# Kernel tuning notes

Measured on AMD Instinct MI355X. Metric: run time of the kernel, lower is better.

Reference implementation:

```python
import jax, jax.numpy as jnp
import numpy as np

S, D, M, K, H = 4096, 768, 1024, 32, 8
DH = D // H  # 96
CTX = 10
EPS_LN = 1e-5
EPS_COS = 1e-8


def setup_inputs() -> dict:
    key = jax.random.key(0)
    ks = jax.random.split(key, 30)
    sc = 0.02
    n = lambda k, shp: jax.random.normal(k, shp, jnp.float32) * sc
    inp = {
        "text_embeddings": jax.random.normal(ks[0], (1, S, D), jnp.float32),
        "candidate_embeddings": jax.random.normal(ks[1], (M, K, D), jnp.float32),
        "mention_starts": jax.random.randint(ks[2], (M,), 0, S - 16),
        "span_lengths": jax.random.randint(ks[3], (M,), 0, 8),
        # relik_reader: Linear(2D->D), ReLU, Linear(D->1)
        "relik_w1": n(ks[4], (2 * D, D)), "relik_b1": jnp.zeros((D,), jnp.float32),
        "relik_w2": n(ks[5], (D, 1)), "relik_b2": jnp.zeros((1,), jnp.float32),
        # TransformerEncoderLayer (post-norm, relu, nhead=8, ffn=4D)
        "wq": n(ks[6], (D, D)), "bq": jnp.zeros((D,), jnp.float32),
        "wk": n(ks[7], (D, D)), "bk": jnp.zeros((D,), jnp.float32),
        "wv": n(ks[8], (D, D)), "bv": jnp.zeros((D,), jnp.float32),
        "wo": n(ks[9], (D, D)), "bo": jnp.zeros((D,), jnp.float32),
        "ln1_g": jnp.ones((D,), jnp.float32), "ln1_b": jnp.zeros((D,), jnp.float32),
        "ffn_w1": n(ks[10], (D, 4 * D)), "ffn_b1": jnp.zeros((4 * D,), jnp.float32),
        "ffn_w2": n(ks[11], (4 * D, D)), "ffn_b2": jnp.zeros((D,), jnp.float32),
        "ln2_g": jnp.ones((D,), jnp.float32), "ln2_b": jnp.zeros((D,), jnp.float32),
        # unirel_interaction: Linear(2D->D), ReLU, Linear(D->D)
        "uni_w1": n(ks[12], (2 * D, D)), "uni_b1": jnp.zeros((D,), jnp.float32),
        "uni_w2": n(ks[13], (D, D)), "uni_b2": jnp.zeros((D,), jnp.float32),
    }
    return inp


def _ln(x, g, b):
    mu = jnp.mean(x, -1, keepdims=True)
    var = jnp.mean(jnp.square(x - mu), -1, keepdims=True)
    return (x - mu) * jax.lax.rsqrt(var + EPS_LN) * g + b


def reference(text_embeddings, candidate_embeddings, mention_starts, span_lengths,
              relik_w1, relik_b1, relik_w2, relik_b2,
              wq, bq, wk, bk, wv, bv, wo, bo,
              ln1_g, ln1_b, ffn_w1, ffn_b1, ffn_w2, ffn_b2, ln2_g, ln2_b,
              uni_w1, uni_b1, uni_w2, uni_b2):
    txt = text_embeddings[0]                               # [S, D]
    seq = txt.shape[0]
    csum = jnp.concatenate([jnp.zeros((1, txt.shape[1]), txt.dtype),
                            jnp.cumsum(txt, axis=0)], axis=0)  # [S+1, D]
    ends = mention_starts + span_lengths
    # mean over [start, end] inclusive
    m_len = (span_lengths + 1).astype(txt.dtype)
    mention = (csum[ends + 1] - csum[mention_starts]) / m_len[:, None]  # [M, D]
    # context mean over [c_start, c_end) exclusive, as in original slicing
    c_start = jnp.maximum(0, mention_starts - CTX)
    c_end = jnp.minimum(seq - 1, ends + CTX)
    ctx = (csum[c_end] - csum[c_start]) / (c_end - c_start).astype(txt.dtype)[:, None]

    cand = candidate_embeddings                            # [M, K, D]
    mk = jnp.broadcast_to(mention[:, None, :], cand.shape) # [M, K, D]

    # relik score: MLP on [mention; candidate]
    cat_mc = jnp.concatenate([mk, cand], axis=-1)          # [M, K, 2D]
    h = jax.nn.relu(cat_mc @ relik_w1 + relik_b1)
    relik = (h @ relik_w2 + relik_b2)[..., 0]              # [M, K]

    # 2-token transformer encoder layer over stack([mention, candidate])
    x = jnp.stack([mk, cand], axis=2)                      # [M, K, 2, D]
    q = (x @ wq + bq).reshape(M, K, 2, H, DH)
    k_ = (x @ wk + bk).reshape(M, K, 2, H, DH)
    v = (x @ wv + bv).reshape(M, K, 2, H, DH)
    scores = jnp.einsum("mkqhd,mkvhd->mkhqv", q, k_) / jnp.sqrt(jnp.float32(DH))
    attn = jax.nn.softmax(scores, axis=-1)
    o = jnp.einsum("mkhqv,mkvhd->mkqhd", attn, v).reshape(M, K, 2, D)
    x1 = _ln(x + (o @ wo + bo), ln1_g, ln1_b)
    f = jax.nn.relu(x1 @ ffn_w1 + ffn_b1) @ ffn_w2 + ffn_b2
    x2 = _ln(x1 + f, ln2_g, ln2_b)                         # [M, K, 2, D]
    e0, e1 = x2[..., 0, :], x2[..., 1, :]
    n0 = jnp.maximum(jnp.linalg.norm(e0, axis=-1), EPS_COS)
    n1 = jnp.maximum(jnp.linalg.norm(e1, axis=-1), EPS_COS)
    atg = jnp.sum(e0 * e1, axis=-1) / (n0 * n1)            # [M, K]

    # unirel: MLP on [context; candidate], sigmoid of mean
    ck = jnp.broadcast_to(ctx[:, None, :], cand.shape)
    cat_cc = jnp.concatenate([ck, cand], axis=-1)
    inter = jax.nn.relu(cat_cc @ uni_w1 + uni_b1) @ uni_w2 + uni_b2
    unirel = jax.nn.sigmoid(jnp.mean(inter, axis=-1))      # [M, K]

    return jnp.stack([relik, atg, unirel], axis=0)         # [3, M, K]
```

## Files before the change

### kernel.cpp

```cpp
#include <hip/hip_runtime.h>
#include <math.h>

#define S_LEN 4096
#define D_DIM 768
#define M_CNT 1024
#define K_CNT 32
#define MK_CNT 32768
#define DH_DIM 96
#define CTX_W 10

typedef __bf16 bf16_t;
typedef bf16_t bf16x8 __attribute__((ext_vector_type(8)));
typedef float f32x4 __attribute__((ext_vector_type(4)));
typedef float f32x16 __attribute__((ext_vector_type(16)));
typedef int i32x4 __attribute__((ext_vector_type(4)));
typedef int i32x8 __attribute__((ext_vector_type(8)));

__device__ __forceinline__ float block_reduce_sum(float v, float* sbuf) {
#pragma unroll
    for (int off = 32; off; off >>= 1) v += __shfl_down(v, off);
    __syncthreads();
    int wave = threadIdx.x >> 6;
    int lane = threadIdx.x & 63;
    if (lane == 0) sbuf[wave] = v;
    __syncthreads();
    return sbuf[0] + sbuf[1] + sbuf[2] + sbuf[3];
}

template<int OUT_BF16, int RELU>
__global__ __launch_bounds__(256, 2) void gemm_mfma(
    const bf16_t* __restrict__ A, const bf16_t* __restrict__ Bt,
    const float* __restrict__ bias, void* __restrict__ C,
    int Kd, int N, int nx, int ny)
{
    __shared__ bf16_t As[128 * 64];
    __shared__ bf16_t Bs[128 * 64];
    const int tid = threadIdx.x;
    const int w = tid >> 6, l = tid & 63;
    int per = 8 * nx;
    int g = blockIdx.x / per, rr = blockIdx.x % per;
    int gs = ny - g * 8; if (gs > 8) gs = 8;
    const int row0 = (g * 8 + rr % gs) * 128, col0 = (rr / gs) * 128;

    const int srow = w * 8 + (l >> 3);
    const int gchunk = (l & 7) ^ ((l >> 3) & 7);
    const bf16_t* gA = A + (size_t)(row0 + srow) * Kd + gchunk * 8;
    const bf16_t* gB = Bt + (size_t)(col0 + srow) * Kd + gchunk * 8;

    const int wm = w >> 1, wn = w & 1;
    f32x4 acc[4][4] = {};

    for (int k0 = 0; k0 < Kd; k0 += 64) {
#pragma unroll
        for (int c = 0; c < 4; ++c) {
            __builtin_amdgcn_global_load_lds(
                (const __attribute__((address_space(1))) void*)(gA + (size_t)(c * 32) * Kd + k0),
                (__attribute__((address_space(3))) void*)(As + (c * 256 + w * 64) * 8), 16, 0, 0);
            __builtin_amdgcn_global_load_lds(
                (const __attribute__((address_space(1))) void*)(gB + (size_t)(c * 32) * Kd + k0),
                (__attribute__((address_space(3))) void*)(Bs + (c * 256 + w * 64) * 8), 16, 0, 0);
        }
        __syncthreads();
#pragma unroll
        for (int ks = 0; ks < 2; ++ks) {
            bf16x8 af[4], bfr[4];
#pragma unroll
            for (int i = 0; i < 4; ++i) {
                int arow = wm * 64 + i * 16 + (l & 15);
                int slot = (ks * 4 + (l >> 4)) ^ (l & 7);
                af[i] = *(const bf16x8*)(As + arow * 64 + slot * 8);
                int brow = wn * 64 + i * 16 + (l & 15);
                bfr[i] = *(const bf16x8*)(Bs + brow * 64 + slot * 8);
            }
#pragma unroll
            for (int i = 0; i < 4; ++i)
#pragma unroll
                for (int j = 0; j < 4; ++j)
                    acc[i][j] = __builtin_amdgcn_mfma_f32_16x16x32_bf16(af[i], bfr[j], acc[i][j], 0, 0, 0);
        }
        __syncthreads();
    }

#pragma unroll
    for (int i = 0; i < 4; ++i) {
        int row = row0 + wm * 64 + i * 16 + (l >> 4) * 4;
#pragma unroll
        for (int j = 0; j < 4; ++j) {
            int col = col0 + wn * 64 + j * 16 + (l & 15);
            float bv = bias ? bias[col] : 0.f;
#pragma unroll
            for (int r = 0; r < 4; ++r) {
                float v = acc[i][j][r] + bv;
                if (RELU) v = fmaxf(v, 0.f);
                if (OUT_BF16) ((bf16_t*)C)[(size_t)(row + r) * N + col] = (bf16_t)v;
                else          ((float*)C)[(size_t)(row + r) * N + col] = v;
            }
        }
    }
}

static inline void launch_gemm(const bf16_t* A, const bf16_t* Bt, const float* bias, void* C,
                               int rows, int Kd, int N, bool relu, bool outbf, hipStream_t st) {
    int nx = N / 128, ny = rows / 128;
    dim3 grid(nx * ny);
    if (outbf) {
        if (relu) gemm_mfma<1, 1><<<grid, 256, 0, st>>>(A, Bt, bias, C, Kd, N, nx, ny);
        else      gemm_mfma<1, 0><<<grid, 256, 0, st>>>(A, Bt, bias, C, Kd, N, nx, ny);
    } else {
        if (relu) gemm_mfma<0, 1><<<grid, 256, 0, st>>>(A, Bt, bias, C, Kd, N, nx, ny);
        else      gemm_mfma<0, 0><<<grid, 256, 0, st>>>(A, Bt, bias, C, Kd, N, nx, ny);
    }
}

template<int OMODE, int RELU>
__global__ __launch_bounds__(256, 2) void gemm_fp8(
    const unsigned char* __restrict__ A, const unsigned char* __restrict__ Bt,
    const float* __restrict__ bias, void* __restrict__ C,
    int Kd, int N, int nx, int ny)
{
    __shared__ unsigned char As[128 * 128];
    __shared__ unsigned char Bs[128 * 128];
    const int tid = threadIdx.x;
    const int w = tid >> 6, l = tid & 63;
    int per = 8 * nx;
    int g = blockIdx.x / per, rrb = blockIdx.x % per;
    int gs = ny - g * 8; if (gs > 8) gs = 8;
    const int row0 = (g * 8 + rrb % gs) * 128, col0 = (rrb / gs) * 128;
    const int wm = w >> 1, wn = w & 1;
    const int SA = 0x7F7F7F7F;

    const int srow = w * 8 + (l >> 3);
    const int gch = (l & 7) ^ ((l >> 3) & 7);
    const unsigned char* gA = A + (size_t)(row0 + srow) * Kd + gch * 16;
    const unsigned char* gB = Bt + (size_t)(col0 + srow) * Kd + gch * 16;

    f32x16 acc[2][2] = {};

    for (int k0 = 0; k0 < Kd; k0 += 128) {
#pragma unroll
        for (int q = 0; q < 4; ++q) {
            __builtin_amdgcn_global_load_lds(
                (const __attribute__((address_space(1))) void*)(gA + (size_t)(q * 32) * Kd + k0),
                (__attribute__((address_space(3))) void*)(As + (q * 256 + w * 64) * 16), 16, 0, 0);
            __builtin_amdgcn_global_load_lds(
                (const __attribute__((address_space(1))) void*)(gB + (size_t)(q * 32) * Kd + k0),
                (__attribute__((address_space(3))) void*)(Bs + (q * 256 + w * 64) * 16), 16, 0, 0);
        }
        __syncthreads();
#pragma unroll
        for (int s = 0; s < 2; ++s) {
            i32x8 af[2], bfr[2];
            int cb = s * 4 + ((l >> 5) << 1);
#pragma unroll
            for (int i = 0; i < 2; ++i) {
                int row = wm * 64 + i * 32 + (l & 31);
                int sl0 = cb ^ (row & 7);
                int sl1 = (cb + 1) ^ (row & 7);
                i32x4 lo = *(const i32x4*)(As + (row * 8 + sl0) * 16);
                i32x4 hi = *(const i32x4*)(As + (row * 8 + sl1) * 16);
                i32x8 a;
                a[0] = lo[0]; a[1] = lo[1]; a[2] = lo[2]; a[3] = lo[3];
                a[4] = hi[0]; a[5] = hi[1]; a[6] = hi[2]; a[7] = hi[3];
                af[i] = a;
                int colr = wn * 64 + i * 32 + (l & 31);
                int tl0 = cb ^ (colr & 7);
                int tl1 = (cb + 1) ^ (colr & 7);
                lo = *(const i32x4*)(Bs + (colr * 8 + tl0) * 16);
                hi = *(const i32x4*)(Bs + (colr * 8 + tl1) * 16);
                i32x8 b;
                b[0] = lo[0]; b[1] = lo[1]; b[2] = lo[2]; b[3] = lo[3];
                b[4] = hi[0]; b[5] = hi[1]; b[6] = hi[2]; b[7] = hi[3];
                bfr[i] = b;
            }
#pragma unroll
            for (int i = 0; i < 2; ++i)
#pragma unroll
                for (int j = 0; j < 2; ++j)
                    acc[i][j] = __builtin_amdgcn_mfma_scale_f32_32x32x64_f8f6f4(
                        af[i], bfr[j], acc[i][j], 0, 0, 0, SA, 0, SA);
        }
        __syncthreads();
    }

#pragma unroll
    for (int i = 0; i < 2; ++i) {
        int rbase = row0 + wm * 64 + i * 32 + 4 * (l >> 5);
#pragma unroll
        for (int j = 0; j < 2; ++j) {
            int col = col0 + wn * 64 + j * 32 + (l & 31);
            float bv = bias ? bias[col] : 0.f;
#pragma unroll
            for (int reg = 0; reg < 16; ++reg) {
                int row = rbase + (reg & 3) + 8 * (reg >> 2);
                float v = acc[i][j][reg] + bv;
                if (RELU) v = fmaxf(v, 0.f);
                if (OMODE == 1)
                    ((unsigned char*)C)[(size_t)row * N + col] =
                        (unsigned char)(__builtin_amdgcn_cvt_pk_fp8_f32(v, v, 0, false) & 0xff);
                else if (OMODE == 2)
                    ((bf16_t*)C)[(size_t)row * N + col] = (bf16_t)v;
                else
                    ((float*)C)[(size_t)row * N + col] = v;
            }
        }
    }
}

template<int OMODE, int RELU>
static inline void launch_fp8_t(const unsigned char* A, const unsigned char* Bt, const float* bias,
                                void* C, int rows, int Kd, int N, hipStream_t st) {
    int nx = N / 128, ny = rows / 128;
    gemm_fp8<OMODE, RELU><<<dim3(nx * ny), 256, 0, st>>>(A, Bt, bias, C, Kd, N, nx, ny);
}

__global__ __launch_bounds__(256) void transpose_bf16(
    const float* __restrict__ W, bf16_t* __restrict__ Wt, int Kd, int N)
{
    __shared__ float t[32][33];
    int bx = blockIdx.x * 32, by = blockIdx.y * 32;
    int x = threadIdx.x & 31, y = threadIdx.x >> 5;
#pragma unroll
    for (int yy = y; yy < 32; yy += 8) t[yy][x] = W[(size_t)(by + yy) * N + bx + x];
    __syncthreads();
#pragma unroll
    for (int yy = y; yy < 32; yy += 8) Wt[(size_t)(bx + yy) * Kd + by + x] = (bf16_t)t[x][yy];
}

__global__ __launch_bounds__(256) void transpose_fp8(
    const float* __restrict__ W, unsigned char* __restrict__ Wt, int Kd, int N)
{
    __shared__ float t[32][33];
    int bx = blockIdx.x * 32, by = blockIdx.y * 32;
    int x = threadIdx.x & 31, y = threadIdx.x >> 5;
#pragma unroll
    for (int yy = y; yy < 32; yy += 8) t[yy][x] = W[(size_t)(by + yy) * N + bx + x];
    __syncthreads();
    int xg = threadIdx.x & 7, yo = threadIdx.x >> 3;
    int lo = __builtin_amdgcn_cvt_pk_fp8_f32(t[xg * 4 + 0][yo], t[xg * 4 + 1][yo], 0, false);
    int both = __builtin_amdgcn_cvt_pk_fp8_f32(t[xg * 4 + 2][yo], t[xg * 4 + 3][yo], lo, true);
    *(int*)(Wt + (size_t)(bx + yo) * Kd + by + xg * 4) = both;
}

__global__ __launch_bounds__(256) void cvt_bf16(
    const float* __restrict__ x, bf16_t* __restrict__ y, int n4)
{
    int i = blockIdx.x * 256 + threadIdx.x;
    if (i < n4) {
        float4 v = ((const float4*)x)[i];
        bf16_t o4[4] = {(bf16_t)v.x, (bf16_t)v.y, (bf16_t)v.z, (bf16_t)v.w};
        ((uint2*)y)[i] = *(uint2*)o4;
    }
}

__global__ __launch_bounds__(256) void pack_bias5(
    const float* __restrict__ bq, const float* __restrict__ bk,
    const float* __restrict__ bv, float* __restrict__ o)
{
    int i = blockIdx.x * 256 + threadIdx.x;
    if (i >= 3840) return;
    float v = 0.f;
    if (i < 768) v = bq[i];
    else if (i < 1536) v = bk[i - 768];
    else if (i < 2304) v = bv[i - 1536];
    o[i] = v;
}

__global__ __launch_bounds__(256) void spans_kernel(
    const float* __restrict__ txt, const int* __restrict__ starts,
    const int* __restrict__ lens, float* __restrict__ mention,
    bf16_t* __restrict__ mentionb, bf16_t* __restrict__ ctxb)
{
    int m = blockIdx.x;
    int st = starts[m], ln = lens[m];
    int en = st + ln;
    int cs = st - CTX_W; if (cs < 0) cs = 0;
    int ce = en + CTX_W; if (ce > S_LEN - 1) ce = S_LEN - 1;
    int c = threadIdx.x;
    float s0 = 0.f, s1 = 0.f, s2 = 0.f;
    for (int r = st; r <= en; ++r) {
        const float* tr = txt + (size_t)r * D_DIM;
        s0 += tr[c]; s1 += tr[c + 256]; s2 += tr[c + 512];
    }
    float inv = 1.f / (float)(ln + 1);
    float* mp = mention + (size_t)m * D_DIM;
    bf16_t* mb = mentionb + (size_t)m * D_DIM;
    mp[c] = s0 * inv; mp[c + 256] = s1 * inv; mp[c + 512] = s2 * inv;
    mb[c] = (bf16_t)(s0 * inv); mb[c + 256] = (bf16_t)(s1 * inv); mb[c + 512] = (bf16_t)(s2 * inv);

    s0 = 0.f; s1 = 0.f; s2 = 0.f;
    for (int r = cs; r < ce; ++r) {
        const float* tr = txt + (size_t)r * D_DIM;
        s0 += tr[c]; s1 += tr[c + 256]; s2 += tr[c + 512];
    }
    inv = 1.f / (float)(ce - cs);
    bf16_t* cp = ctxb + (size_t)m * D_DIM;
    cp[c] = (bf16_t)(s0 * inv); cp[c + 256] = (bf16_t)(s1 * inv); cp[c + 512] = (bf16_t)(s2 * inv);
}

__global__ __launch_bounds__(256) void w2bar_kernel(
    const float* __restrict__ uni_w2, const float* __restrict__ uni_b2,
    float* __restrict__ w2bar, float* __restrict__ b2bar)
{
    __shared__ float sbuf[4];
    int d = blockIdx.x;
    float s = 0.f;
    if (d < D_DIM) {
        for (int j = threadIdx.x; j < D_DIM; j += 256) s += uni_w2[(size_t)d * D_DIM + j];
        s = block_reduce_sum(s, sbuf);
        if (threadIdx.x == 0) w2bar[d] = s * (1.f / (float)D_DIM);
    } else {
        for (int j = threadIdx.x; j < D_DIM; j += 256) s += uni_b2[j];
        s = block_reduce_sum(s, sbuf);
        if (threadIdx.x == 0) *b2bar = s * (1.f / (float)D_DIM);
    }
}

__global__ __launch_bounds__(512) void attn_kernel(
    const bf16_t* __restrict__ qkvm, const bf16_t* __restrict__ qkvc,
    bf16_t* __restrict__ o, int g0)
{
    int lc = blockIdx.x;
    int gg = g0 + lc;
    int m = gg >> 5;
    int h = threadIdx.x >> 6;
    int lane = threadIdx.x & 63;
    const bf16_t* bm = qkvm + (size_t)m * 3840 + h * DH_DIM;
    const bf16_t* bc = qkvc + (size_t)lc * 3840 + h * DH_DIM;

    float s00 = 0.f, s01 = 0.f, s10 = 0.f, s11 = 0.f;
    for (int d = lane; d < DH_DIM; d += 64) {
        float qmv = (float)bm[d], kmv = (float)bm[d + 768];
        float qcv = (float)bc[d], kcv = (float)bc[d + 768];
        s00 += qmv * kmv; s01 += qmv * kcv; s10 += qcv * kmv; s11 += qcv * kcv;
    }
#pragma unroll
    for (int off = 32; off; off >>= 1) {
        s00 += __shfl_down(s00, off); s01 += __shfl_down(s01, off);
        s10 += __shfl_down(s10, off); s11 += __shfl_down(s11, off);
    }
    s00 = __shfl(s00, 0); s01 = __shfl(s01, 0);
    s10 = __shfl(s10, 0); s11 = __shfl(s11, 0);
    const float sc = 0.1020620726159658f;
    s00 *= sc; s01 *= sc; s10 *= sc; s11 *= sc;
    float m0 = fmaxf(s00, s01), m1 = fmaxf(s10, s11);
    float e00 = expf(s00 - m0), e01 = expf(s01 - m0);
    float e10 = expf(s10 - m1), e11 = expf(s11 - m1);
    float i0 = 1.f / (e00 + e01), i1 = 1.f / (e10 + e11);
    float a00 = e00 * i0, a01 = e01 * i0, a10 = e10 * i1, a11 = e11 * i1;

    bf16_t* o0 = o + ((size_t)lc * 2) * D_DIM + h * DH_DIM;
    bf16_t* o1 = o0 + D_DIM;
    for (int d = lane; d < DH_DIM; d += 64) {
        float vmv = (float)bm[d + 1536], vcv = (float)bc[d + 1536];
        o0[d] = (bf16_t)(a00 * vmv + a01 * vcv);
        o1[d] = (bf16_t)(a10 * vmv + a11 * vcv);
    }
}

__global__ __launch_bounds__(256) void ln1_kernel(
    const bf16_t* __restrict__ x1pre, const float* __restrict__ mention,
    const bf16_t* __restrict__ candb, const float* __restrict__ g,
    const float* __restrict__ b, bf16_t* __restrict__ x1f,
    unsigned char* __restrict__ x1q, int g0)
{
    __shared__ float sbuf[4];
    int r = blockIdx.x;
    int lc = r >> 1, pos = r & 1;
    int gg = g0 + lc, m = gg >> 5;
    int c = threadIdx.x;
    float r0, r1, r2;
    if (pos) {
        const bf16_t* xr = candb + (size_t)gg * D_DIM;
        r0 = (float)xr[c]; r1 = (float)xr[c + 256]; r2 = (float)xr[c + 512];
    } else {
        const float* xr = mention + (size_t)m * D_DIM;
        r0 = xr[c]; r1 = xr[c + 256]; r2 = xr[c + 512];
    }
    const bf16_t* pr = x1pre + (size_t)r * D_DIM;
    float v0 = r0 + (float)pr[c];
    float v1 = r1 + (float)pr[c + 256];
    float v2 = r2 + (float)pr[c + 512];
    float mu = block_reduce_sum(v0 + v1 + v2, sbuf) * (1.f / (float)D_DIM);
    float d0 = v0 - mu, d1 = v1 - mu, d2 = v2 - mu;
    float var = block_reduce_sum(d0 * d0 + d1 * d1 + d2 * d2, sbuf) * (1.f / (float)D_DIM);
    float inv = rsqrtf(var + 1e-5f);
    float o0 = d0 * inv * g[c] + b[c];
    float o1 = d1 * inv * g[c + 256] + b[c + 256];
    float o2 = d2 * inv * g[c + 512] + b[c + 512];
    bf16_t* fp = x1f + (size_t)r * D_DIM;
    fp[c] = (bf16_t)o0; fp[c + 256] = (bf16_t)o1; fp[c + 512] = (bf16_t)o2;
    unsigned char* qp = x1q + (size_t)r * D_DIM;
    qp[c] = (unsigned char)(__builtin_amdgcn_cvt_pk_fp8_f32(o0, o0, 0, false) & 0xff);
    qp[c + 256] = (unsigned char)(__builtin_amdgcn_cvt_pk_fp8_f32(o1, o1, 0, false) & 0xff);
    qp[c + 512] = (unsigned char)(__builtin_amdgcn_cvt_pk_fp8_f32(o2, o2, 0, false) & 0xff);
}

__global__ __launch_bounds__(256) void heads_kernel(
    const bf16_t* __restrict__ x1f, const bf16_t* __restrict__ x2f,
    const float* __restrict__ g2, const float* __restrict__ b2g,
    const float* __restrict__ Ar, const float* __restrict__ Au,
    const bf16_t* __restrict__ qkvc, const float* __restrict__ rw2,
    const float* __restrict__ rb2, const float* __restrict__ w2bar,
    const float* __restrict__ b2bar, float* __restrict__ out, int g0)
{
    __shared__ float sbuf[4];
    int lc = blockIdx.x;
    int gg = g0 + lc, m = gg >> 5;
    int c = threadIdx.x;
    float e[2][3];
#pragma unroll
    for (int rr = 0; rr < 2; ++rr) {
        const bf16_t* x1 = x1f + (size_t)(2 * lc + rr) * D_DIM;
        const bf16_t* x2 = x2f + (size_t)(2 * lc + rr) * D_DIM;
        float v0 = (float)x1[c] + (float)x2[c];
        float v1 = (float)x1[c + 256] + (float)x2[c + 256];
        float v2 = (float)x1[c + 512] + (float)x2[c + 512];
        float mu = block_reduce_sum(v0 + v1 + v2, sbuf) * (1.f / (float)D_DIM);
        float d0 = v0 - mu, d1 = v1 - mu, d2 = v2 - mu;
        float var = block_reduce_sum(d0 * d0 + d1 * d1 + d2 * d2, sbuf) * (1.f / (float)D_DIM);
        float inv = rsqrtf(var + 1e-5f);
        e[rr][0] = d0 * inv * g2[c] + b2g[c];
        e[rr][1] = d1 * inv * g2[c + 256] + b2g[c + 256];
        e[rr][2] = d2 * inv * g2[c + 512] + b2g[c + 512];
    }
    float dd = e[0][0] * e[1][0] + e[0][1] * e[1][1] + e[0][2] * e[1][2];
    float aa = e[0][0] * e[0][0] + e[0][1] * e[0][1] + e[0][2] * e[0][2];
    float bb = e[1][0] * e[1][0] + e[1][1] * e[1][1] + e[1][2] * e[1][2];
    dd = block_reduce_sum(dd, sbuf);
    aa = block_reduce_sum(aa, sbuf);
    bb = block_reduce_sum(bb, sbuf);
    const float* ar = Ar + (size_t)m * D_DIM;
    const bf16_t* br = qkvc + (size_t)lc * 3840 + 2304;
    float rs = fmaxf(ar[c] + (float)br[c], 0.f) * rw2[c]
             + fmaxf(ar[c + 256] + (float)br[c + 256], 0.f) * rw2[c + 256]
             + fmaxf(ar[c + 512] + (float)br[c + 512], 0.f) * rw2[c + 512];
    rs = block_reduce_sum(rs, sbuf);
    const float* au = Au + (size_t)m * D_DIM;
    const bf16_t* bu = qkvc + (size_t)lc * 3840 + 3072;
    float us = fmaxf(au[c] + (float)bu[c], 0.f) * w2bar[c]
             + fmaxf(au[c + 256] + (float)bu[c + 256], 0.f) * w2bar[c + 256]
             + fmaxf(au[c + 512] + (float)bu[c + 512], 0.f) * w2bar[c + 512];
    us = block_reduce_sum(us, sbuf);
    if (threadIdx.x == 0) {
        float n0 = fmaxf(sqrtf(aa), 1e-8f);
        float n1 = fmaxf(sqrtf(bb), 1e-8f);
        out[MK_CNT + gg] = dd / (n0 * n1);
        out[gg] = rs + rb2[0];
        float z = us + *b2bar;
        out[2 * MK_CNT + gg] = 1.f / (1.f + expf(-z));
    }
}

extern "C" void kernel_launch(void* const* d_in, const int* in_sizes, int n_in,
                              void* d_out, int out_size, void* d_ws, size_t ws_size,
                              hipStream_t stream) {
    const float* text     = (const float*)d_in[0];
    const float* cand     = (const float*)d_in[1];
    const int*   starts   = (const int*)d_in[2];
    const int*   lens     = (const int*)d_in[3];
    const float* relik_w1 = (const float*)d_in[4];
    const float* relik_b1 = (const float*)d_in[5];
    const float* relik_w2 = (const float*)d_in[6];
    const float* relik_b2 = (const float*)d_in[7];
    const float* wq = (const float*)d_in[8];
    const float* bq = (const float*)d_in[9];
    const float* wk = (const float*)d_in[10];
    const float* bk = (const float*)d_in[11];
    const float* wv = (const float*)d_in[12];
    const float* bv = (const float*)d_in[13];
    const float* wo = (const float*)d_in[14];
    const float* bo = (const float*)d_in[15];
    const float* ln1_g = (const float*)d_in[16];
    const float* ln1_b = (const float*)d_in[17];
    const float* ffn_w1 = (const float*)d_in[18];
    const float* ffn_b1 = (const float*)d_in[19];
    const float* ffn_w2 = (const float*)d_in[20];
    const float* ffn_b2 = (const float*)d_in[21];
    const float* ln2_g = (const float*)d_in[22];
    const float* ln2_b = (const float*)d_in[23];
    const float* uni_w1 = (const float*)d_in[24];
    const float* uni_b1 = (const float*)d_in[25];
    const float* uni_w2 = (const float*)d_in[26];
    const float* uni_b2 = (const float*)d_in[27];
    float* out = (float*)d_out;

    const size_t MD = (size_t)M_CNT * D_DIM;
    const size_t DD = (size_t)D_DIM * D_DIM;

    size_t fixed_f = 21300000;
    int NC = 32768;
    while (NC > 128 && (fixed_f + (size_t)NC * 6912) * 4 > ws_size) NC >>= 1;
    const size_t NCD = (size_t)NC * D_DIM;

    float* p = (float*)d_ws;
    float* mention = p; p += MD;
    float* Ar      = p; p += MD;
    float* Au      = p; p += MD;
    float* bqkv5   = p; p += 3840;
    float* w2bar   = p; p += 768;
    float* b2bar   = p; p += 64;
    bf16_t* mentionb = (bf16_t*)p; p += MD / 2;
    bf16_t* ctxb     = (bf16_t*)p; p += MD / 2;
    bf16_t* qkvm     = (bf16_t*)p; p += (size_t)M_CNT * 3840 / 2;
    bf16_t* wcandT   = (bf16_t*)p; p += (size_t)3840 * 768 / 2;
    bf16_t* woT      = (bf16_t*)p; p += DD / 2;
    bf16_t* relikAT  = (bf16_t*)p; p += DD / 2;
    bf16_t* uniAT    = (bf16_t*)p; p += DD / 2;
    unsigned char* w1q = (unsigned char*)p; p += (size_t)3072 * 768 / 4;
    unsigned char* w2q = (unsigned char*)p; p += (size_t)3072 * 768 / 4;
    bf16_t* candb    = (bf16_t*)p; p += (size_t)MK_CNT * D_DIM / 2;
    bf16_t* qkvcb = (bf16_t*)p; p += (size_t)NC * 3840 / 2;
    bf16_t* obuf  = (bf16_t*)p; p += 2 * NCD / 2;
    bf16_t* x1pre = (bf16_t*)p; p += 2 * NCD / 2;
    bf16_t* x1f   = (bf16_t*)p; p += 2 * NCD / 2;
    bf16_t* x2f   = (bf16_t*)p; p += 2 * NCD / 2;
    unsigned char* x1q = (unsigned char*)p; p += 2 * NCD / 4;
    unsigned char* hb  = (unsigned char*)p; p += (size_t)2 * NC * 3072 / 4;

    dim3 t768(768 / 32, 768 / 32);
    transpose_bf16<<<t768, 256, 0, stream>>>(wq, wcandT, 768, 768);
    transpose_bf16<<<t768, 256, 0, stream>>>(wk, wcandT + DD, 768, 768);
    transpose_bf16<<<t768, 256, 0, stream>>>(wv, wcandT + 2 * DD, 768, 768);
    transpose_bf16<<<t768, 256, 0, stream>>>(relik_w1 + DD, wcandT + 3 * DD, 768, 768);
    transpose_bf16<<<t768, 256, 0, stream>>>(uni_w1 + DD, wcandT + 4 * DD, 768, 768);
    transpose_bf16<<<t768, 256, 0, stream>>>(wo, woT, 768, 768);
    transpose_bf16<<<t768, 256, 0, stream>>>(relik_w1, relikAT, 768, 768);
    transpose_bf16<<<t768, 256, 0, stream>>>(uni_w1, uniAT, 768, 768);
    transpose_fp8<<<dim3(3072 / 32, 768 / 32), 256, 0, stream>>>(ffn_w1, w1q, 768, 3072);
    transpose_fp8<<<dim3(768 / 32, 3072 / 32), 256, 0, stream>>>(ffn_w2, w2q, 3072, 768);
    pack_bias5<<<15, 256, 0, stream>>>(bq, bk, bv, bqkv5);
    w2bar_kernel<<<D_DIM + 1, 256, 0, stream>>>(uni_w2, uni_b2, w2bar, b2bar);
    cvt_bf16<<<(MK_CNT * D_DIM / 4 + 255) / 256, 256, 0, stream>>>(cand, candb, MK_CNT * D_DIM / 4);

    spans_kernel<<<M_CNT, 256, 0, stream>>>(text, starts, lens, mention, mentionb, ctxb);
    launch_gemm(mentionb, wcandT, bqkv5, qkvm, M_CNT, 768, 3840, false, true, stream);
    launch_gemm(mentionb, relikAT, relik_b1, Ar, M_CNT, 768, 768, false, false, stream);
    launch_gemm(ctxb, uniAT, uni_b1, Au, M_CNT, 768, 768, false, false, stream);

    int nch = MK_CNT / NC;
    for (int c = 0; c < nch; ++c) {
        int g0 = c * NC;
        const bf16_t* cc = candb + (size_t)g0 * D_DIM;
        launch_gemm(cc, wcandT, bqkv5, qkvcb, NC, 768, 3840, false, true, stream);

        attn_kernel<<<NC, 512, 0, stream>>>(qkvm, qkvcb, obuf, g0);

        launch_gemm(obuf, woT, bo, x1pre, 2 * NC, 768, 768, false, true, stream);
        ln1_kernel<<<2 * NC, 256, 0, stream>>>(x1pre, mention, candb,
                                               ln1_g, ln1_b, x1f, x1q, g0);

        launch_fp8_t<1, 1>(x1q, w1q, ffn_b1, hb, 2 * NC, 768, 3072, stream);
        launch_fp8_t<2, 0>(hb, w2q, ffn_b2, x2f, 2 * NC, 3072, 768, stream);

        heads_kernel<<<NC, 256, 0, stream>>>(x1f, x2f, ln2_g, ln2_b, Ar, Au, qkvcb,
                                             relik_w2, relik_b2, w2bar, b2bar, out, g0);
    }
}
```

Before: 1.330 ms.

## Move QKV and output-projection GEMMs to FP8 and split candidate GEMM

Quantizes the Q/K/V and Wo weights, the candidate and mention embeddings, and the attention output to FP8. The QKV projections and the output projection now use the FP8 MFMA GEMM instead of the bf16 one. The former fused 3840-wide candidate GEMM is split into an FP8 2304-wide QKV GEMM and a bf16 1536-wide relik/unirel GEMM, which the heads kernel reads from its own buffer. This aims to halve operand bandwidth and raise MFMA throughput on the attention path, at the cost of lower precision in attention scores and outputs, plus an extra GEMM launch and an FP8 candidate copy.

```diff
diff --git a/kernel.cpp b/kernel.cpp
--- a/kernel.cpp
+++ b/kernel.cpp
@@ -25,6 +25,10 @@
     if (lane == 0) sbuf[wave] = v;
     __syncthreads();
     return sbuf[0] + sbuf[1] + sbuf[2] + sbuf[3];
+}
+
+__device__ __forceinline__ unsigned char to_fp8(float v) {
+    return (unsigned char)(__builtin_amdgcn_cvt_pk_fp8_f32(v, v, 0, false) & 0xff);
 }
 
 template<int OUT_BF16, int RELU>
@@ -195,8 +199,7 @@
                 float v = acc[i][j][reg] + bv;
                 if (RELU) v = fmaxf(v, 0.f);
                 if (OMODE == 1)
-                    ((unsigned char*)C)[(size_t)row * N + col] =
-                        (unsigned char)(__builtin_amdgcn_cvt_pk_fp8_f32(v, v, 0, false) & 0xff);
+                    ((unsigned char*)C)[(size_t)row * N + col] = to_fp8(v);
                 else if (OMODE == 2)
                     ((bf16_t*)C)[(size_t)row * N + col] = (bf16_t)v;
                 else
@@ -241,34 +244,34 @@
     *(int*)(Wt + (size_t)(bx + yo) * Kd + by + xg * 4) = both;
 }
 
-__global__ __launch_bounds__(256) void cvt_bf16(
-    const float* __restrict__ x, bf16_t* __restrict__ y, int n4)
+__global__ __launch_bounds__(256) void cvt_cand(
+    const float* __restrict__ x, bf16_t* __restrict__ yb,
+    unsigned char* __restrict__ yq, int n4)
 {
     int i = blockIdx.x * 256 + threadIdx.x;
     if (i < n4) {
         float4 v = ((const float4*)x)[i];
         bf16_t o4[4] = {(bf16_t)v.x, (bf16_t)v.y, (bf16_t)v.z, (bf16_t)v.w};
-        ((uint2*)y)[i] = *(uint2*)o4;
-    }
-}
-
-__global__ __launch_bounds__(256) void pack_bias5(
+        ((uint2*)yb)[i] = *(uint2*)o4;
+        int lo = __builtin_amdgcn_cvt_pk_fp8_f32(v.x, v.y, 0, false);
+        int both = __builtin_amdgcn_cvt_pk_fp8_f32(v.z, v.w, lo, true);
+        ((int*)yq)[i] = both;
+    }
+}
+
+__global__ __launch_bounds__(256) void pack_bias(
     const float* __restrict__ bq, const float* __restrict__ bk,
     const float* __restrict__ bv, float* __restrict__ o)
 {
     int i = blockIdx.x * 256 + threadIdx.x;
-    if (i >= 3840) return;
-    float v = 0.f;
-    if (i < 768) v = bq[i];
-    else if (i < 1536) v = bk[i - 768];
-    else if (i < 2304) v = bv[i - 1536];
-    o[i] = v;
+    if (i < 768) { o[i] = bq[i]; o[i + 768] = bk[i]; o[i + 1536] = bv[i]; }
 }
 
 __global__ __launch_bounds__(256) void spans_kernel(
     const float* __restrict__ txt, const int* __restrict__ starts,
     const int* __restrict__ lens, float* __restrict__ mention,
-    bf16_t* __restrict__ mentionb, bf16_t* __restrict__ ctxb)
+    unsigned char* __restrict__ mentionq, bf16_t* __restrict__ mentionb,
+    bf16_t* __restrict__ ctxb)
 {
     int m = blockIdx.x;
     int st = starts[m], ln = lens[m];
@@ -282,10 +285,13 @@
         s0 += tr[c]; s1 += tr[c + 256]; s2 += tr[c + 512];
     }
     float inv = 1.f / (float)(ln + 1);
+    float v0 = s0 * inv, v1 = s1 * inv, v2 = s2 * inv;
     float* mp = mention + (size_t)m * D_DIM;
     bf16_t* mb = mentionb + (size_t)m * D_DIM;
-    mp[c] = s0 * inv; mp[c + 256] = s1 * inv; mp[c + 512] = s2 * inv;
-    mb[c] = (bf16_t)(s0 * inv); mb[c + 256] = (bf16_t)(s1 * inv); mb[c + 512] = (bf16_t)(s2 * inv);
+    unsigned char* mq = mentionq + (size_t)m * D_DIM;
+    mp[c] = v0; mp[c + 256] = v1; mp[c + 512] = v2;
+    mb[c] = (bf16_t)v0; mb[c + 256] = (bf16_t)v1; mb[c + 512] = (bf16_t)v2;
+    mq[c] = to_fp8(v0); mq[c + 256] = to_fp8(v1); mq[c + 512] = to_fp8(v2);
 
     s0 = 0.f; s1 = 0.f; s2 = 0.f;
     for (int r = cs; r < ce; ++r) {
@@ -317,15 +323,15 @@
 
 __global__ __launch_bounds__(512) void attn_kernel(
     const bf16_t* __restrict__ qkvm, const bf16_t* __restrict__ qkvc,
-    bf16_t* __restrict__ o, int g0)
+    unsigned char* __restrict__ o, int g0)
 {
     int lc = blockIdx.x;
     int gg = g0 + lc;
     int m = gg >> 5;
     int h = threadIdx.x >> 6;
     int lane = threadIdx.x & 63;
-    const bf16_t* bm = qkvm + (size_t)m * 3840 + h * DH_DIM;
-    const bf16_t* bc = qkvc + (size_t)lc * 3840 + h * DH_DIM;
+    const bf16_t* bm = qkvm + (size_t)m * 2304 + h * DH_DIM;
+    const bf16_t* bc = qkvc + (size_t)lc * 2304 + h * DH_DIM;
 
     float s00 = 0.f, s01 = 0.f, s10 = 0.f, s11 = 0.f;
     for (int d = lane; d < DH_DIM; d += 64) {
@@ -348,12 +354,12 @@
     float i0 = 1.f / (e00 + e01), i1 = 1.f / (e10 + e11);
     float a00 = e00 * i0, a01 = e01 * i0, a10 = e10 * i1, a11 = e11 * i1;
 
-    bf16_t* o0 = o + ((size_t)lc * 2) * D_DIM + h * DH_DIM;
-    bf16_t* o1 = o0 + D_DIM;
+    unsigned char* o0 = o + ((size_t)lc * 2) * D_DIM + h * DH_DIM;
+    unsigned char* o1 = o0 + D_DIM;
     for (int d = lane; d < DH_DIM; d += 64) {
         float vmv = (float)bm[d + 1536], vcv = (float)bc[d + 1536];
-        o0[d] = (bf16_t)(a00 * vmv + a01 * vcv);
-        o1[d] = (bf16_t)(a10 * vmv + a11 * vcv);
+        o0[d] = to_fp8(a00 * vmv + a01 * vcv);
+        o1[d] = to_fp8(a10 * vmv + a11 * vcv);
     }
 }
 
@@ -390,16 +396,14 @@
     bf16_t* fp = x1f + (size_t)r * D_DIM;
     fp[c] = (bf16_t)o0; fp[c + 256] = (bf16_t)o1; fp[c + 512] = (bf16_t)o2;
     unsigned char* qp = x1q + (size_t)r * D_DIM;
-    qp[c] = (unsigned char)(__builtin_amdgcn_cvt_pk_fp8_f32(o0, o0, 0, false) & 0xff);
-    qp[c + 256] = (unsigned char)(__builtin_amdgcn_cvt_pk_fp8_f32(o1, o1, 0, false) & 0xff);
-    qp[c + 512] = (unsigned char)(__builtin_amdgcn_cvt_pk_fp8_f32(o2, o2, 0, false) & 0xff);
+    qp[c] = to_fp8(o0); qp[c + 256] = to_fp8(o1); qp[c + 512] = to_fp8(o2);
 }
 
 __global__ __launch_bounds__(256) void heads_kernel(
     const bf16_t* __restrict__ x1f, const bf16_t* __restrict__ x2f,
     const float* __restrict__ g2, const float* __restrict__ b2g,
     const float* __restrict__ Ar, const float* __restrict__ Au,
-    const bf16_t* __restrict__ qkvc, const float* __restrict__ rw2,
+    const bf16_t* __restrict__ ru, const float* __restrict__ rw2,
     const float* __restrict__ rb2, const float* __restrict__ w2bar,
     const float* __restrict__ b2bar, float* __restrict__ out, int g0)
 {
@@ -430,13 +434,13 @@
     aa = block_reduce_sum(aa, sbuf);
     bb = block_reduce_sum(bb, sbuf);
     const float* ar = Ar + (size_t)m * D_DIM;
-    const bf16_t* br = qkvc + (size_t)lc * 3840 + 2304;
+    const bf16_t* br = ru + (size_t)lc * 1536;
     float rs = fmaxf(ar[c] + (float)br[c], 0.f) * rw2[c]
              + fmaxf(ar[c + 256] + (float)br[c + 256], 0.f) * rw2[c + 256]
              + fmaxf(ar[c + 512] + (float)br[c + 512], 0.f) * rw2[c + 512];
     rs = block_reduce_sum(rs, sbuf);
     const float* au = Au + (size_t)m * D_DIM;
-    const bf16_t* bu = qkvc + (size_t)lc * 3840 + 3072;
+    const bf16_t* bu = br + 768;
     float us = fmaxf(au[c] + (float)bu[c], 0.f) * w2bar[c]
              + fmaxf(au[c + 256] + (float)bu[c + 256], 0.f) * w2bar[c + 256]
              + fmaxf(au[c + 512] + (float)bu[c + 512], 0.f) * w2bar[c + 512];
@@ -487,30 +491,34 @@
     const size_t MD = (size_t)M_CNT * D_DIM;
     const size_t DD = (size_t)D_DIM * D_DIM;
 
-    size_t fixed_f = 21300000;
+    size_t fixed_f = 26500000;
     int NC = 32768;
-    while (NC > 128 && (fixed_f + (size_t)NC * 6912) * 4 > ws_size) NC >>= 1;
+    while (NC > 128 && (fixed_f + (size_t)NC * 6528) * 4 > ws_size) NC >>= 1;
     const size_t NCD = (size_t)NC * D_DIM;
 
     float* p = (float*)d_ws;
     float* mention = p; p += MD;
     float* Ar      = p; p += MD;
     float* Au      = p; p += MD;
-    float* bqkv5   = p; p += 3840;
+    float* bqkv    = p; p += 2304;
     float* w2bar   = p; p += 768;
     float* b2bar   = p; p += 64;
     bf16_t* mentionb = (bf16_t*)p; p += MD / 2;
     bf16_t* ctxb     = (bf16_t*)p; p += MD / 2;
-    bf16_t* qkvm     = (bf16_t*)p; p += (size_t)M_CNT * 3840 / 2;
-    bf16_t* wcandT   = (bf16_t*)p; p += (size_t)3840 * 768 / 2;
-    bf16_t* woT      = (bf16_t*)p; p += DD / 2;
+    unsigned char* mentionq = (unsigned char*)p; p += MD / 4;
+    bf16_t* qkvm     = (bf16_t*)p; p += (size_t)M_CNT * 2304 / 2;
     bf16_t* relikAT  = (bf16_t*)p; p += DD / 2;
     bf16_t* uniAT    = (bf16_t*)p; p += DD / 2;
+    bf16_t* wruT     = (bf16_t*)p; p += 2 * DD / 2;
+    unsigned char* wqkvq = (unsigned char*)p; p += 3 * DD / 4;
+    unsigned char* woq   = (unsigned char*)p; p += DD / 4;
     unsigned char* w1q = (unsigned char*)p; p += (size_t)3072 * 768 / 4;
     unsigned char* w2q = (unsigned char*)p; p += (size_t)3072 * 768 / 4;
     bf16_t* candb    = (bf16_t*)p; p += (size_t)MK_CNT * D_DIM / 2;
-    bf16_t* qkvcb = (bf16_t*)p; p += (size_t)NC * 3840 / 2;
-    bf16_t* obuf  = (bf16_t*)p; p += 2 * NCD / 2;
+    unsigned char* candq = (unsigned char*)p; p += (size_t)MK_CNT * D_DIM / 4;
+    bf16_t* qkvcb = (bf16_t*)p; p += (size_t)NC * 2304 / 2;
+    bf16_t* rucb  = (bf16_t*)p; p += (size_t)NC * 1536 / 2;
+    unsigned char* obuf = (unsigned char*)p; p += 2 * NCD / 4;
     bf16_t* x1pre = (bf16_t*)p; p += 2 * NCD / 2;
     bf16_t* x1f   = (bf16_t*)p; p += 2 * NCD / 2;
     bf16_t* x2f   = (bf16_t*)p; p += 2 * NCD / 2;
@@ -518,41 +526,41 @@
     unsigned char* hb  = (unsigned char*)p; p += (size_t)2 * NC * 3072 / 4;
 
     dim3 t768(768 / 32, 768 / 32);
-    transpose_bf16<<<t768, 256, 0, stream>>>(wq, wcandT, 768, 768);
-    transpose_bf16<<<t768, 256, 0, stream>>>(wk, wcandT + DD, 768, 768);
-    transpose_bf16<<<t768, 256, 0, stream>>>(wv, wcandT + 2 * DD, 768, 768);
-    transpose_bf16<<<t768, 256, 0, stream>>>(relik_w1 + DD, wcandT + 3 * DD, 768, 768);
-    transpose_bf16<<<t768, 256, 0, stream>>>(uni_w1 + DD, wcandT + 4 * DD, 768, 768);
-    transpose_bf16<<<t768, 256, 0, stream>>>(wo, woT, 768, 768);
+    transpose_fp8<<<t768, 256, 0, stream>>>(wq, wqkvq, 768, 768);
+    transpose_fp8<<<t768, 256, 0, stream>>>(wk, wqkvq + DD, 768, 768);
+    transpose_fp8<<<t768, 256, 0, stream>>>(wv, wqkvq + 2 * DD, 768, 768);
+    transpose_fp8<<<t768, 256, 0, stream>>>(wo, woq, 768, 768);
+    transpose_bf16<<<t768, 256, 0, stream>>>(relik_w1 + DD, wruT, 768, 768);
+    transpose_bf16<<<t768, 256, 0, stream>>>(uni_w1 + DD, wruT + DD, 768, 768);
     transpose_bf16<<<t768, 256, 0, stream>>>(relik_w1, relikAT, 768, 768);
     transpose_bf16<<<t768, 256, 0, stream>>>(uni_w1, uniAT, 768, 768);
     transpose_fp8<<<dim3(3072 / 32, 768 / 32), 256, 0, stream>>>(ffn_w1, w1q, 768, 3072);
     transpose_fp8<<<dim3(768 / 32, 3072 / 32), 256, 0, stream>>>(ffn_w2, w2q, 3072, 768);
-    pack_bias5<<<15, 256, 0, stream>>>(bq, bk, bv, bqkv5);
+    pack_bias<<<3, 256, 0, stream>>>(bq, bk, bv, bqkv);
     w2bar_kernel<<<D_DIM + 1, 256, 0, stream>>>(uni_w2, uni_b2, w2bar, b2bar);
-    cvt_bf16<<<(MK_CNT * D_DIM / 4 + 255) / 256, 256, 0, stream>>>(cand, candb, MK_CNT * D_DIM / 4);
-
-    spans_kernel<<<M_CNT, 256, 0, stream>>>(text, starts, lens, mention, mentionb, ctxb);
-    launch_gemm(mentionb, wcandT, bqkv5, qkvm, M_CNT, 768, 3840, false, true, stream);
+    cvt_cand<<<(MK_CNT * D_DIM / 4 + 255) / 256, 256, 0, stream>>>(cand, candb, candq, MK_CNT * D_DIM / 4);
+
+    spans_kernel<<<M_CNT, 256, 0, stream>>>(text, starts, lens, mention, mentionq, mentionb, ctxb);
+    launch_fp8_t<2, 0>(mentionq, wqkvq, bqkv, qkvm, M_CNT, 768, 2304, stream);
     launch_gemm(mentionb, relikAT, relik_b1, Ar, M_CNT, 768, 768, false, false, stream);
     launch_gemm(ctxb, uniAT, uni_b1, Au, M_CNT, 768, 768, false, false, stream);
 
     int nch = MK_CNT / NC;
     for (int c = 0; c < nch; ++c) {
         int g0 = c * NC;
-        const bf16_t* cc = candb + (size_t)g0 * D_DIM;
-        launch_gemm(cc, wcandT, bqkv5, qkvcb, NC, 768, 3840, false, true, stream);
+        launch_fp8_t<2, 0>(candq + (size_t)g0 * D_DIM, wqkvq, bqkv, qkvcb, NC, 768, 2304, stream);
+        launch_gemm(candb + (size_t)g0 * D_DIM, wruT, nullptr, rucb, NC, 768, 1536, false, true, stream);
 
         attn_kernel<<<NC, 512, 0, stream>>>(qkvm, qkvcb, obuf, g0);
 
-        launch_gemm(obuf, woT, bo, x1pre, 2 * NC, 768, 768, false, true, stream);
+        launch_fp8_t<2, 0>(obuf, woq, bo, x1pre, 2 * NC, 768, 768, stream);
         ln1_kernel<<<2 * NC, 256, 0, stream>>>(x1pre, mention, candb,
                                                ln1_g, ln1_b, x1f, x1q, g0);
 
         launch_fp8_t<1, 1>(x1q, w1q, ffn_b1, hb, 2 * NC, 768, 3072, stream);
         launch_fp8_t<2, 0>(hb, w2q, ffn_b2, x2f, 2 * NC, 3072, 768, stream);
 
-        heads_kernel<<<NC, 256, 0, stream>>>(x1f, x2f, ln2_g, ln2_b, Ar, Au, qkvcb,
+        heads_kernel<<<NC, 256, 0, stream>>>(x1f, x2f, ln2_g, ln2_b, Ar, Au, rucb,
                                              relik_w2, relik_b2, w2bar, b2bar, out, g0);
     }
 }
```

Result: faster. 1.247 ms (-6.2%).
